# Performance work log

Hardware: AMD Instinct MI355X
Metric: run time of the kernel (lower is better)

## Reference

```python
import jax, jax.numpy as jnp
import numpy as np
import math

D = 512
H = 8
DH = D // H
B, T = 4, 2048


def _poly(x, coeffs):
    # iterative-power polynomial eval, same products as the Vandermonde matmul
    acc = coeffs[0] * jnp.ones_like(x)
    p = jnp.ones_like(x)
    for i in range(1, coeffs.shape[0]):
        p = p * x
        acc = acc + coeffs[i] * p
    return acc


def _exp_fn(x, exp_c):
    return jnp.maximum(_poly(x, exp_c), 1e-8)


def _softmax(x, exp_c):
    x = x - jnp.max(x, axis=-1, keepdims=True)
    e = _exp_fn(x, exp_c)
    return e / jnp.sum(e, axis=-1, keepdims=True)


def _gelu(x, gelu_c):
    return _poly(jnp.clip(x, -4.0, 4.0), gelu_c)


def _layernorm(x, gamma, beta):
    mean = jnp.mean(x, axis=-1, keepdims=True)
    var = jnp.mean(x * x, axis=-1, keepdims=True) - mean * mean
    v = var + 1e-5
    y = jnp.full_like(v, 0.5)
    for _ in range(3):  # Newton iterations for rsqrt
        y = y * (3.0 - v * y * y) * 0.5
    return (x - mean) * y * gamma + beta


def setup_inputs() -> dict:
    key = jax.random.key(0)
    ks = jax.random.split(key, 8)
    x = jax.random.normal(ks[0], (B, T, D), dtype=jnp.float32)
    s = 0.02
    Wq = jax.random.normal(ks[1], (D, D), dtype=jnp.float32) * s
    Wk = jax.random.normal(ks[2], (D, D), dtype=jnp.float32) * s
    Wv = jax.random.normal(ks[3], (D, D), dtype=jnp.float32) * s
    Wo = jax.random.normal(ks[4], (D, D), dtype=jnp.float32) * s
    W1 = jax.random.normal(ks[5], (D, 4 * D), dtype=jnp.float32) * s
    W2 = jax.random.normal(ks[6], (4 * D, D), dtype=jnp.float32) * s
    g1 = jnp.ones((D,), jnp.float32); b1 = jnp.zeros((D,), jnp.float32)
    g2 = jnp.ones((D,), jnp.float32); b2 = jnp.zeros((D,), jnp.float32)
    # GELU degree-7 least-squares fit on [-4,4]
    x_fit = jnp.linspace(-4.0, 4.0, 1000)
    y_fit = 0.5 * x_fit * (1.0 + jax.scipy.special.erf(x_fit / math.sqrt(2.0)))
    V = x_fit[:, None] ** jnp.arange(8)[None, :]
    gelu_c = jnp.linalg.lstsq(V, y_fit)[0].astype(jnp.float32)
    # exp Taylor coeffs degree 6
    exp_c = jnp.array([1.0 / math.factorial(i) for i in range(7)], dtype=jnp.float32)
    return dict(x=x, Wq=Wq, Wk=Wk, Wv=Wv, Wo=Wo, W1=W1, W2=W2,
                g1=g1, b1=b1, g2=g2, b2=b2, gelu_c=gelu_c, exp_c=exp_c)


def reference(x, Wq, Wk, Wv, Wo, W1, W2, g1, b1, g2, b2, gelu_c, exp_c):
    Bn, Tn, Dn = x.shape
    q = (x @ Wq).reshape(Bn, Tn, H, DH).transpose(0, 2, 1, 3)  # [B,H,T,dh]
    k = (x @ Wk).reshape(Bn, Tn, H, DH).transpose(0, 2, 1, 3)
    v = (x @ Wv).reshape(Bn, Tn, H, DH).transpose(0, 2, 1, 3)
    scores = jnp.einsum('bhqd,bhkd->bhqk', q, k) / math.sqrt(DH)
    attn = _softmax(scores, exp_c)
    out = jnp.einsum('bhqk,bhkd->bhqd', attn, v).transpose(0, 2, 1, 3).reshape(Bn, Tn, Dn)
    out = out @ Wo
    h = _layernorm(x + out, g1, b1)
    ffn = _gelu(h @ W1, gelu_c) @ W2
    return _layernorm(h + ffn, g2, b2)
```

## Files before the change

kernel.cpp:

```cpp
#include <hip/hip_runtime.h>
#include <hip/hip_bf16.h>

typedef __bf16 bf16_t;
typedef __bf16 bf16x8 __attribute__((ext_vector_type(8)));
typedef float f32x4 __attribute__((ext_vector_type(4)));

#define MFMA16(a, b, c) __builtin_amdgcn_mfma_f32_16x16x32_bf16((a), (b), (c), 0, 0, 0)

__device__ __forceinline__ void gl_lds16(const bf16_t* g, bf16_t* l) {
  __builtin_amdgcn_global_load_lds(
      (const __attribute__((address_space(1))) void*)g,
      (__attribute__((address_space(3))) void*)l, 16, 0, 0);
}

__device__ __forceinline__ unsigned pack_bf16(float a, float b) {
  union { bf16_t h[2]; unsigned u; } c;
  c.h[0] = (bf16_t)a; c.h[1] = (bf16_t)b;
  return c.u;
}

__global__ __launch_bounds__(256) void k_prep(
    const float* __restrict__ x, bf16_t* __restrict__ x_bf,
    const float* __restrict__ Wq, const float* __restrict__ Wk,
    const float* __restrict__ Wv, const float* __restrict__ Wo,
    const float* __restrict__ W1, const float* __restrict__ W2,
    bf16_t* __restrict__ WqkvT, bf16_t* __restrict__ WoT,
    bf16_t* __restrict__ W1T, bf16_t* __restrict__ W2T) {
  __shared__ float tile[64][65];
  int bid = blockIdx.x, tid = threadIdx.x;
  if (bid < 4096) {
    int i = bid * 256 + tid;
    float4 f = ((const float4*)x)[i];
    union { bf16_t h[4]; uint2 u; } cv;
    cv.h[0] = (bf16_t)f.x; cv.h[1] = (bf16_t)f.y;
    cv.h[2] = (bf16_t)f.z; cv.h[3] = (bf16_t)f.w;
    ((uint2*)x_bf)[i] = cv.u;
    return;
  }
  int t = bid - 4096;
  const float* W; bf16_t* WT; int K, N, idx, gx;
  if (t < 64)       { W = Wq; WT = WqkvT;                      K = 512;  N = 512;  idx = t;       gx = 8;  }
  else if (t < 128) { W = Wk; WT = WqkvT + (size_t)512 * 512;  K = 512;  N = 512;  idx = t - 64;  gx = 8;  }
  else if (t < 192) { W = Wv; WT = WqkvT + (size_t)1024 * 512; K = 512;  N = 512;  idx = t - 128; gx = 8;  }
  else if (t < 256) { W = Wo; WT = WoT;                        K = 512;  N = 512;  idx = t - 192; gx = 8;  }
  else if (t < 512) { W = W1; WT = W1T;                        K = 512;  N = 2048; idx = t - 256; gx = 8;  }
  else              { W = W2; WT = W2T;                        K = 2048; N = 512;  idx = t - 512; gx = 32; }
  int bk = (idx % gx) * 64, bn = (idx / gx) * 64;
  int tx = tid & 63, ty = tid >> 6;
  for (int i = ty; i < 64; i += 4)
    tile[i][tx] = W[(size_t)(bk + i) * N + bn + tx];
  __syncthreads();
  for (int i = ty; i < 64; i += 4)
    WT[(size_t)(bn + i) * K + bk + tx] = (bf16_t)tile[tx][i];
}

template <int MODE, int BM>
__global__ __launch_bounds__(256) void k_gemm_bt(
    const bf16_t* __restrict__ A, const bf16_t* __restrict__ Bt,
    float* __restrict__ Cf, bf16_t* __restrict__ Cb,
    bf16_t* __restrict__ Cb2, bf16_t* __restrict__ Cb3,
    int M, int N, int K, const float* __restrict__ coef) {
  __shared__ __align__(16) bf16_t As[2][BM * 32];
  __shared__ __align__(16) bf16_t Bs[2][128 * 32];
  constexpr int NF = (BM == 128) ? 4 : 2;
  int tid = threadIdx.x;
  int lane = tid & 63, wave = tid >> 6;
  int bm = blockIdx.x * BM, bn = blockIdx.y * 128;
  int wr = (BM == 128) ? (wave >> 1) * 64 : 0;
  int wc = (BM == 128) ? (wave & 1) * 64 : wave * 32;
  int lr = lane & 15, lk = (lane >> 4) * 8;
  int srow = tid >> 2, scol = (tid & 3) * 8;

  f32x4 zero = {0.f, 0.f, 0.f, 0.f};
  f32x4 acc[4][NF];
#pragma unroll
  for (int m = 0; m < 4; ++m)
#pragma unroll
    for (int n = 0; n < NF; ++n) acc[m][n] = zero;

  const bf16_t* pA = A + (size_t)(bm + srow) * K + scol;
  const bf16_t* pB = Bt + (size_t)(bn + srow) * K + scol;

  auto STAGE = [&](int buf, int k0) {
    bf16_t* lA = &As[buf][tid * 8];
    bf16_t* lB = &Bs[buf][tid * 8];
    gl_lds16(pA + k0, lA);
    if (BM == 128) gl_lds16(pA + (size_t)64 * K + k0, lA + 2048);
    gl_lds16(pB + k0, lB);
    gl_lds16(pB + (size_t)64 * K + k0, lB + 2048);
  };

  STAGE(0, 0);
  __syncthreads();
  int buf = 0;
  for (int k0 = 0; k0 < K; k0 += 32) {
    if (k0 + 32 < K) STAGE(buf ^ 1, k0 + 32);
    bf16x8 a[4], b[NF];
#pragma unroll
    for (int m = 0; m < 4; ++m) a[m] = *(const bf16x8*)&As[buf][(wr + m * 16 + lr) * 32 + lk];
#pragma unroll
    for (int n = 0; n < NF; ++n) b[n] = *(const bf16x8*)&Bs[buf][(wc + n * 16 + lr) * 32 + lk];
    __builtin_amdgcn_s_setprio(1);
#pragma unroll
    for (int m = 0; m < 4; ++m)
#pragma unroll
      for (int n = 0; n < NF; ++n)
        acc[m][n] = MFMA16(a[m], b[n], acc[m][n]);
    __builtin_amdgcn_s_setprio(0);
    __syncthreads();
    buf ^= 1;
  }

  float c8[8];
  if (MODE == 4) {
#pragma unroll
    for (int i = 0; i < 8; ++i) c8[i] = coef[i];
  }
  int rbase = (lane >> 4) * 4;
#pragma unroll
  for (int m = 0; m < 4; ++m) {
#pragma unroll
    for (int n = 0; n < NF; ++n) {
#pragma unroll
      for (int r = 0; r < 4; ++r) {
        int gm = bm + wr + m * 16 + rbase + r;
        int gn = bn + wc + n * 16 + lr;
        float v = acc[m][n][r];
        if (MODE == 0) {
          Cf[(size_t)gm * N + gn] = v;
        } else if (MODE == 4) {
          float xx = fminf(fmaxf(v, -4.f), 4.f);
          float p = c8[0], pw = 1.f;
#pragma unroll
          for (int i = 1; i < 8; ++i) { pw *= xx; p += c8[i] * pw; }
          Cb[(size_t)gm * N + gn] = (bf16_t)p;
        } else {
          int mat = gn >> 9, col = gn & 511;
          int b_ = gm >> 11, t_ = gm & 2047, h_ = col >> 6, d_ = col & 63;
          if (mat == 0) {
            Cb[(((size_t)b_ * 8 + h_) * 2048 + t_) * 64 + d_] = (bf16_t)(v * 0.125f);
          } else if (mat == 1) {
            int dsw = d_ ^ ((t_ & 7) << 3);
            Cb2[(((size_t)b_ * 8 + h_) * 2048 + t_) * 64 + dsw] = (bf16_t)v;
          } else {
            int tw = t_ & 63;
            int j = (((tw >> 2) & 3) << 1) | ((tw >> 4) & 1);
            int phys = (((tw & 32) << 1) + (j << 3) + ((tw & 3) << 1)) ^ ((d_ & 7) << 4);
            size_t e = ((((size_t)b_ * 8 + h_) * 64 + d_) * 4096 +
                        (size_t)(t_ >> 6) * 128 + phys) >> 1;
            Cb3[e] = (bf16_t)v;
          }
        }
      }
    }
  }
}

__global__ __launch_bounds__(256) void k_attn(
    const bf16_t* __restrict__ qb, const bf16_t* __restrict__ kb,
    const bf16_t* __restrict__ vtb, bf16_t* __restrict__ ob,
    const float* __restrict__ exp_c) {
  __shared__ __align__(16) bf16_t Ks[3][64 * 64];
  __shared__ __align__(16) bf16_t Vs[2][64 * 64];
  int tid = threadIdx.x, lane = tid & 63, wave = tid >> 6;
  int b0 = blockIdx.x;
  int bid = (b0 & 7) * 128 + (b0 >> 3);
  int qt = bid & 31, bh = bid >> 5;
  const size_t bho = (size_t)bh * (2048 * 64);
  const bf16_t* Q = qb + bho + (size_t)qt * 64 * 64;
  const bf16_t* Kp = kb + bho;
  const bf16_t* Vp = vtb + bho;
  int lr = lane & 15, lg = lane >> 4;

  bf16x8 qa[2];
#pragma unroll
  for (int h = 0; h < 2; ++h)
    qa[h] = *(const bf16x8*)&Q[(wave * 16 + lr) * 64 + h * 32 + lg * 8];

  float ec[7];
#pragma unroll
  for (int i = 0; i < 7; ++i) ec[i] = exp_c[i];

  auto STAGE_K = [&](int buf, int kt) {
    bf16_t* lk = &Ks[buf][tid * 8];
    const bf16_t* gk = Kp + (size_t)kt * 4096 + tid * 8;
    gl_lds16(gk, lk);
    gl_lds16(gk + 2048, lk + 2048);
  };
  auto STAGE_V = [&](int buf, int kt) {
    bf16_t* lv = &Vs[buf][tid * 8];
    const bf16_t* gv = Vp + (size_t)(tid >> 3) * 2048 + kt * 64 + (tid & 7) * 8;
    gl_lds16(gv, lv);
    gl_lds16(gv + (size_t)32 * 2048, lv + 2048);
  };

  f32x4 zero = {0.f, 0.f, 0.f, 0.f};
  auto qk_tile = [&](const char* kbase, f32x4* sout) {
    __builtin_amdgcn_s_setprio(1);
#pragma unroll
    for (int n = 0; n < 4; ++n) {
      int row = n * 16 + lr, sw = (row & 7) << 4;
      bf16x8 kb0 = *(const bf16x8*)(kbase + ((row * 128 + lg * 16) ^ sw));
      bf16x8 kb1 = *(const bf16x8*)(kbase + ((row * 128 + 64 + lg * 16) ^ sw));
      sout[n] = MFMA16(kb1, qa[1], MFMA16(kb0, qa[0], zero));
    }
    __builtin_amdgcn_s_setprio(0);
  };

  f32x4 s[4], s2[4];
  f32x4 oacc[4];
#pragma unroll
  for (int n = 0; n < 4; ++n) oacc[n] = zero;
  float rsum = 0.f;

  STAGE_K(0, 0);
  STAGE_K(1, 1);
  STAGE_V(0, 0);
  __syncthreads();
  qk_tile((const char*)Ks[0], s);

  for (int kt = 0; kt < 32; ++kt) {
    if (kt < 30) STAGE_K((kt + 2) % 3, kt + 2);
    if (kt < 31) STAGE_V((kt + 1) & 1, kt + 1);
    if (kt < 31) qk_tile((const char*)Ks[(kt + 1) % 3], s2);
    unsigned pk[4][2];
#pragma unroll
    for (int n = 0; n < 4; ++n) {
      float pf[4];
#pragma unroll
      for (int r = 0; r < 4; ++r) {
        float xv = s[n][r];
        float p = ec[6];
#pragma unroll
        for (int i = 5; i >= 0; --i) p = __builtin_fmaf(p, xv, ec[i]);
        p = fmaxf(p, 1e-8f);
        rsum += p;
        pf[r] = p;
      }
      pk[n][0] = pack_bf16(pf[0], pf[1]);
      pk[n][1] = pack_bf16(pf[2], pf[3]);
    }
    union { unsigned u[4]; bf16x8 v; } pa0, pa1;
    pa0.u[0] = pk[0][0]; pa0.u[1] = pk[0][1]; pa0.u[2] = pk[1][0]; pa0.u[3] = pk[1][1];
    pa1.u[0] = pk[2][0]; pa1.u[1] = pk[2][1]; pa1.u[2] = pk[3][0]; pa1.u[3] = pk[3][1];
    const char* vbase = (const char*)Vs[kt & 1];
    __builtin_amdgcn_s_setprio(1);
#pragma unroll
    for (int dd = 0; dd < 4; ++dd) {
      int row = dd * 16 + lr, sw = (row & 7) << 4;
      bf16x8 v0 = *(const bf16x8*)(vbase + ((row * 128 + lg * 16) ^ sw));
      bf16x8 v1 = *(const bf16x8*)(vbase + ((row * 128 + 64 + lg * 16) ^ sw));
      oacc[dd] = MFMA16(pa1.v, v1, MFMA16(pa0.v, v0, oacc[dd]));
    }
    __builtin_amdgcn_s_setprio(0);
    __syncthreads();
    if (kt < 31) {
#pragma unroll
      for (int n = 0; n < 4; ++n) s[n] = s2[n];
    }
  }
  rsum += __shfl_xor(rsum, 16);
  rsum += __shfl_xor(rsum, 32);
  float rs4[4];
#pragma unroll
  for (int r = 0; r < 4; ++r) rs4[r] = __shfl(rsum, lg * 4 + r);

  int b_ = bh >> 3, h_ = bh & 7;
#pragma unroll
  for (int dd = 0; dd < 4; ++dd)
#pragma unroll
    for (int r = 0; r < 4; ++r) {
      int t_ = qt * 64 + wave * 16 + lg * 4 + r;
      int d_ = dd * 16 + lr;
      float val = oacc[dd][r] / rs4[r];
      ob[(((size_t)b_ * 2048 + t_) * 8 + h_) * 64 + d_] = (bf16_t)val;
    }
}

__global__ __launch_bounds__(256) void k_ln(
    const float* __restrict__ xa, const float* __restrict__ xb,
    const float* __restrict__ gamma, const float* __restrict__ beta,
    float* __restrict__ outf, bf16_t* __restrict__ outb) {
  int row = blockIdx.x * 4 + (threadIdx.x >> 6);
  int lane = threadIdx.x & 63;
  const float* pa = xa + (size_t)row * 512;
  const float* pb = xb + (size_t)row * 512;
  float4 a0 = ((const float4*)pa)[lane];
  float4 a1 = ((const float4*)pa)[lane + 64];
  float4 b0 = ((const float4*)pb)[lane];
  float4 b1 = ((const float4*)pb)[lane + 64];
  float x[8] = {a0.x + b0.x, a0.y + b0.y, a0.z + b0.z, a0.w + b0.w,
                a1.x + b1.x, a1.y + b1.y, a1.z + b1.z, a1.w + b1.w};
  float s = 0.f, sq = 0.f;
#pragma unroll
  for (int i = 0; i < 8; ++i) { s += x[i]; sq += x[i] * x[i]; }
#pragma unroll
  for (int off = 1; off < 64; off <<= 1) {
    s += __shfl_xor(s, off);
    sq += __shfl_xor(sq, off);
  }
  float mean = s * (1.f / 512.f);
  float var = sq * (1.f / 512.f) - mean * mean;
  float v = var + 1e-5f;
  float y = 0.5f;
#pragma unroll
  for (int it = 0; it < 3; ++it) y = y * (3.0f - v * y * y) * 0.5f;

  float4 g0 = ((const float4*)gamma)[lane];
  float4 g1 = ((const float4*)gamma)[lane + 64];
  float4 e0 = ((const float4*)beta)[lane];
  float4 e1 = ((const float4*)beta)[lane + 64];
  float o[8];
  o[0] = (x[0] - mean) * y * g0.x + e0.x;
  o[1] = (x[1] - mean) * y * g0.y + e0.y;
  o[2] = (x[2] - mean) * y * g0.z + e0.z;
  o[3] = (x[3] - mean) * y * g0.w + e0.w;
  o[4] = (x[4] - mean) * y * g1.x + e1.x;
  o[5] = (x[5] - mean) * y * g1.y + e1.y;
  o[6] = (x[6] - mean) * y * g1.z + e1.z;
  o[7] = (x[7] - mean) * y * g1.w + e1.w;
  float* po = outf + (size_t)row * 512;
  ((float4*)po)[lane]      = make_float4(o[0], o[1], o[2], o[3]);
  ((float4*)po)[lane + 64] = make_float4(o[4], o[5], o[6], o[7]);
  if (outb) {
    bf16_t* pq = outb + (size_t)row * 512;
    union { bf16_t h[4]; uint2 u; } c0, c1;
    c0.h[0] = (bf16_t)o[0]; c0.h[1] = (bf16_t)o[1]; c0.h[2] = (bf16_t)o[2]; c0.h[3] = (bf16_t)o[3];
    c1.h[0] = (bf16_t)o[4]; c1.h[1] = (bf16_t)o[5]; c1.h[2] = (bf16_t)o[6]; c1.h[3] = (bf16_t)o[7];
    ((uint2*)pq)[lane]      = c0.u;
    ((uint2*)pq)[lane + 64] = c1.u;
  }
}

extern "C" void kernel_launch(void* const* d_in, const int* in_sizes, int n_in,
                              void* d_out, int out_size, void* d_ws, size_t ws_size,
                              hipStream_t stream) {
  const float* x      = (const float*)d_in[0];
  const float* Wq     = (const float*)d_in[1];
  const float* Wk     = (const float*)d_in[2];
  const float* Wv     = (const float*)d_in[3];
  const float* Wo     = (const float*)d_in[4];
  const float* W1     = (const float*)d_in[5];
  const float* W2     = (const float*)d_in[6];
  const float* g1     = (const float*)d_in[7];
  const float* b1     = (const float*)d_in[8];
  const float* g2     = (const float*)d_in[9];
  const float* b2     = (const float*)d_in[10];
  const float* gelu_c = (const float*)d_in[11];
  const float* exp_c  = (const float*)d_in[12];

  const int M = 8192;
  const size_t actBF = (size_t)M * 512 * 2;
  char* p = (char*)d_ws;
  auto carve = [&](size_t bytes) {
    void* r = (void*)p;
    p += (bytes + 255) & ~(size_t)255;
    return r;
  };
  bf16_t* x_bf   = (bf16_t*)carve(actBF);
  bf16_t* q_bf   = (bf16_t*)carve(actBF);
  bf16_t* k_bf   = (bf16_t*)carve(actBF);
  bf16_t* vT_bf  = (bf16_t*)carve(actBF);
  bf16_t* o_bf   = (bf16_t*)carve(actBF);
  bf16_t* h_bf   = (bf16_t*)carve(actBF);
  bf16_t* WqkvT  = (bf16_t*)carve((size_t)1536 * 512 * 2);
  bf16_t* WoT    = (bf16_t*)carve(512 * 512 * 2);
  bf16_t* W1T    = (bf16_t*)carve(512 * 2048 * 2);
  bf16_t* W2T    = (bf16_t*)carve(512 * 2048 * 2);
  bf16_t* g_bf   = (bf16_t*)carve((size_t)M * 2048 * 2);
  float*  proj   = (float*)carve((size_t)M * 512 * 4);
  float*  h_f    = (float*)carve((size_t)M * 512 * 4);
  float*  f2     = proj;

  k_prep<<<4864, 256, 0, stream>>>(x, x_bf, Wq, Wk, Wv, Wo, W1, W2,
                                   WqkvT, WoT, W1T, W2T);

  k_gemm_bt<5, 128><<<dim3(64, 12), 256, 0, stream>>>(
      x_bf, WqkvT, nullptr, q_bf, k_bf, vT_bf, M, 1536, 512, nullptr);

  k_attn<<<1024, 256, 0, stream>>>(q_bf, k_bf, vT_bf, o_bf, exp_c);

  k_gemm_bt<0, 64><<<dim3(128, 4), 256, 0, stream>>>(
      o_bf, WoT, proj, nullptr, nullptr, nullptr, M, 512, 512, nullptr);

  k_ln<<<2048, 256, 0, stream>>>(x, proj, g1, b1, h_f, h_bf);

  k_gemm_bt<4, 128><<<dim3(64, 16), 256, 0, stream>>>(
      h_bf, W1T, nullptr, g_bf, nullptr, nullptr, M, 2048, 512, gelu_c);

  k_gemm_bt<0, 64><<<dim3(128, 4), 256, 0, stream>>>(
      g_bf, W2T, f2, nullptr, nullptr, nullptr, M, 512, 2048, nullptr);

  k_ln<<<2048, 256, 0, stream>>>(h_f, f2, g2, b2, (float*)d_out, nullptr);
}
```

Measured before the change: 201.5 us.

## Load K/V fragments directly from global into registers, drop LDS staging

The attention kernel no longer stages K and V tiles through shared memory with async global-to-LDS copies and block barriers. Each lane now loads its MFMA fragments straight from global memory into registers and prefetches the next tile after each use, so the LDS swizzle is removed from the QKV projection epilogue. This removes LDS traffic and __syncthreads, but each wave re-reads K/V from global/L2 with no sharing across the four waves, and there is less latency hiding. The fmaxf clamp on the polynomial exp is also dropped, which changes numerics for very negative scores.

```diff
diff --git a/kernel.cpp b/kernel.cpp
--- a/kernel.cpp
+++ b/kernel.cpp
@@ -140,12 +140,11 @@
           if (mat == 0) {
             Cb[(((size_t)b_ * 8 + h_) * 2048 + t_) * 64 + d_] = (bf16_t)(v * 0.125f);
           } else if (mat == 1) {
-            int dsw = d_ ^ ((t_ & 7) << 3);
-            Cb2[(((size_t)b_ * 8 + h_) * 2048 + t_) * 64 + dsw] = (bf16_t)v;
+            Cb2[(((size_t)b_ * 8 + h_) * 2048 + t_) * 64 + d_] = (bf16_t)v;
           } else {
             int tw = t_ & 63;
             int j = (((tw >> 2) & 3) << 1) | ((tw >> 4) & 1);
-            int phys = (((tw & 32) << 1) + (j << 3) + ((tw & 3) << 1)) ^ ((d_ & 7) << 4);
+            int phys = ((tw & 32) << 1) + (j << 3) + ((tw & 3) << 1);
             size_t e = ((((size_t)b_ * 8 + h_) * 64 + d_) * 4096 +
                         (size_t)(t_ >> 6) * 128 + phys) >> 1;
             Cb3[e] = (bf16_t)v;
@@ -160,8 +159,6 @@
     const bf16_t* __restrict__ qb, const bf16_t* __restrict__ kb,
     const bf16_t* __restrict__ vtb, bf16_t* __restrict__ ob,
     const float* __restrict__ exp_c) {
-  __shared__ __align__(16) bf16_t Ks[3][64 * 64];
-  __shared__ __align__(16) bf16_t Vs[2][64 * 64];
   int tid = threadIdx.x, lane = tid & 63, wave = tid >> 6;
   int b0 = blockIdx.x;
   int bid = (b0 & 7) * 128 + (b0 >> 3);
@@ -181,48 +178,38 @@
 #pragma unroll
   for (int i = 0; i < 7; ++i) ec[i] = exp_c[i];
 
-  auto STAGE_K = [&](int buf, int kt) {
-    bf16_t* lk = &Ks[buf][tid * 8];
-    const bf16_t* gk = Kp + (size_t)kt * 4096 + tid * 8;
-    gl_lds16(gk, lk);
-    gl_lds16(gk + 2048, lk + 2048);
-  };
-  auto STAGE_V = [&](int buf, int kt) {
-    bf16_t* lv = &Vs[buf][tid * 8];
-    const bf16_t* gv = Vp + (size_t)(tid >> 3) * 2048 + kt * 64 + (tid & 7) * 8;
-    gl_lds16(gv, lv);
-    gl_lds16(gv + (size_t)32 * 2048, lv + 2048);
-  };
+  bf16x8 kf[8], vf[8];
+  const bf16_t* kfb = Kp + (size_t)(lr)*64 + lg * 8;
+  const bf16_t* vfb = Vp + (size_t)(lr)*2048 + lg * 8;
+#pragma unroll
+  for (int n = 0; n < 4; ++n)
+#pragma unroll
+    for (int h = 0; h < 2; ++h) {
+      kf[2 * n + h] = *(const bf16x8*)(kfb + n * 1024 + h * 32);
+      vf[2 * n + h] = *(const bf16x8*)(vfb + (size_t)n * 16 * 2048 + h * 32);
+    }
 
   f32x4 zero = {0.f, 0.f, 0.f, 0.f};
-  auto qk_tile = [&](const char* kbase, f32x4* sout) {
-    __builtin_amdgcn_s_setprio(1);
-#pragma unroll
-    for (int n = 0; n < 4; ++n) {
-      int row = n * 16 + lr, sw = (row & 7) << 4;
-      bf16x8 kb0 = *(const bf16x8*)(kbase + ((row * 128 + lg * 16) ^ sw));
-      bf16x8 kb1 = *(const bf16x8*)(kbase + ((row * 128 + 64 + lg * 16) ^ sw));
-      sout[n] = MFMA16(kb1, qa[1], MFMA16(kb0, qa[0], zero));
-    }
-    __builtin_amdgcn_s_setprio(0);
-  };
-
-  f32x4 s[4], s2[4];
   f32x4 oacc[4];
 #pragma unroll
   for (int n = 0; n < 4; ++n) oacc[n] = zero;
   float rsum = 0.f;
 
-  STAGE_K(0, 0);
-  STAGE_K(1, 1);
-  STAGE_V(0, 0);
-  __syncthreads();
-  qk_tile((const char*)Ks[0], s);
-
   for (int kt = 0; kt < 32; ++kt) {
-    if (kt < 30) STAGE_K((kt + 2) % 3, kt + 2);
-    if (kt < 31) STAGE_V((kt + 1) & 1, kt + 1);
-    if (kt < 31) qk_tile((const char*)Ks[(kt + 1) % 3], s2);
+    f32x4 s[4];
+    __builtin_amdgcn_s_setprio(1);
+#pragma unroll
+    for (int n = 0; n < 4; ++n)
+      s[n] = MFMA16(kf[2 * n + 1], qa[1], MFMA16(kf[2 * n], qa[0], zero));
+    __builtin_amdgcn_s_setprio(0);
+    if (kt < 31) {
+      const bf16_t* kp = kfb + (size_t)(kt + 1) * 4096;
+#pragma unroll
+      for (int n = 0; n < 4; ++n)
+#pragma unroll
+        for (int h = 0; h < 2; ++h)
+          kf[2 * n + h] = *(const bf16x8*)(kp + n * 1024 + h * 32);
+    }
     unsigned pk[4][2];
 #pragma unroll
     for (int n = 0; n < 4; ++n) {
@@ -233,7 +220,6 @@
         float p = ec[6];
 #pragma unroll
         for (int i = 5; i >= 0; --i) p = __builtin_fmaf(p, xv, ec[i]);
-        p = fmaxf(p, 1e-8f);
         rsum += p;
         pf[r] = p;
       }
@@ -243,20 +229,18 @@
     union { unsigned u[4]; bf16x8 v; } pa0, pa1;
     pa0.u[0] = pk[0][0]; pa0.u[1] = pk[0][1]; pa0.u[2] = pk[1][0]; pa0.u[3] = pk[1][1];
     pa1.u[0] = pk[2][0]; pa1.u[1] = pk[2][1]; pa1.u[2] = pk[3][0]; pa1.u[3] = pk[3][1];
-    const char* vbase = (const char*)Vs[kt & 1];
     __builtin_amdgcn_s_setprio(1);
 #pragma unroll
-    for (int dd = 0; dd < 4; ++dd) {
-      int row = dd * 16 + lr, sw = (row & 7) << 4;
-      bf16x8 v0 = *(const bf16x8*)(vbase + ((row * 128 + lg * 16) ^ sw));
-      bf16x8 v1 = *(const bf16x8*)(vbase + ((row * 128 + 64 + lg * 16) ^ sw));
-      oacc[dd] = MFMA16(pa1.v, v1, MFMA16(pa0.v, v0, oacc[dd]));
-    }
+    for (int dd = 0; dd < 4; ++dd)
+      oacc[dd] = MFMA16(pa1.v, vf[2 * dd + 1], MFMA16(pa0.v, vf[2 * dd], oacc[dd]));
     __builtin_amdgcn_s_setprio(0);
-    __syncthreads();
     if (kt < 31) {
-#pragma unroll
-      for (int n = 0; n < 4; ++n) s[n] = s2[n];
+      const bf16_t* vp = vfb + (kt + 1) * 64;
+#pragma unroll
+      for (int dd = 0; dd < 4; ++dd)
+#pragma unroll
+        for (int h = 0; h < 2; ++h)
+          vf[2 * dd + h] = *(const bf16x8*)(vp + (size_t)dd * 16 * 2048 + h * 32);
     }
   }
   rsum += __shfl_xor(rsum, 16);
```

Result: slower. 361.3 us (+79.3%).
